# Performance work log

Measured on AMD Instinct MI355X. Metric: run time of the kernel, lower is better.

Reference implementation:

```python
import jax, jax.numpy as jnp
import numpy as np

OBS_SIZE = 128
ACTION_SIZE = 10
B = 64
T = 512
FEAT = 512          # HIDDEN_SIZE
H = 256             # HIDDEN_MEMORY_SIZE


def setup_inputs() -> dict:
    key = jax.random.key(0)
    ks = jax.random.split(key, 16)
    s = 0.05
    return {
        "obs": jax.random.normal(ks[0], (B, T, OBS_SIZE), jnp.float32),
        "action": jax.random.randint(ks[1], (B * T,), 0, ACTION_SIZE, jnp.int64 if jax.config.jax_enable_x64 else jnp.int32),
        "masks": jax.random.randint(ks[2], (B, T - 1), 0, 2, jnp.int32),
        "old_hidden_memory": jax.random.normal(ks[3], (B, 1, H), jnp.float32),
        # fnn: Linear(obs_size, 512) + ReLU
        "W1": jax.random.normal(ks[4], (FEAT, OBS_SIZE), jnp.float32) * s,
        "b1": jnp.zeros((FEAT,), jnp.float32),
        # GRU weights, PyTorch layout: gates ordered (r, z, n)
        "W_ih": jax.random.normal(ks[5], (3 * H, FEAT), jnp.float32) * s,
        "W_hh": jax.random.normal(ks[6], (3 * H, H), jnp.float32) * s,
        "b_ih": jnp.zeros((3 * H,), jnp.float32),
        "b_hh": jnp.zeros((3 * H,), jnp.float32),
        # actor / critic heads
        "Wa": jax.random.normal(ks[7], (ACTION_SIZE, H), jnp.float32) * s,
        "ba": jnp.zeros((ACTION_SIZE,), jnp.float32),
        "Wc": jax.random.normal(ks[8], (1, H), jnp.float32) * s,
        "bc": jnp.zeros((1,), jnp.float32),
    }


def _evaluate_action(obs, old_hidden_memory, W1, b1, W_ih, W_hh, b_ih, b_hh,
                     Wa, ba, Wc, bc, action, masks):
    # feature extractor: Linear + ReLU  [B,T,FEAT]
    feat = jax.nn.relu(jnp.einsum('bto,fo->btf', obs, W1) + b1)

    # Precompute input-side gate projections once: [T,B,3H]
    gx = jnp.einsum('btf,gf->tbg', feat, W_ih) + b_ih

    # mask sequence: prepend a column of ones, per the torch code -> [T,B]
    mask_seq = jnp.concatenate(
        [jnp.ones((1, B), jnp.float32), masks.astype(jnp.float32).T], axis=0)

    h0 = old_hidden_memory[:, 0]  # [B,H]

    def cell(h, inp):
        gx_t, m_t = inp
        h = h * m_t[:, None]                       # episode-reset masking
        gh = h @ W_hh.T + b_hh                     # [B,3H]
        r = jax.nn.sigmoid(gx_t[:, :H] + gh[:, :H])
        z = jax.nn.sigmoid(gx_t[:, H:2 * H] + gh[:, H:2 * H])
        n = jnp.tanh(gx_t[:, 2 * H:] + r * gh[:, 2 * H:])
        h_new = (1.0 - z) * n + z * h
        return h_new, h_new

    _, hs = jax.lax.scan(cell, h0, (gx, mask_seq))  # hs: [T,B,H]
    hs = hs.transpose(1, 0, 2).reshape(B * T, H)    # flatten(end_dim=1)

    logits = hs @ Wa.T + ba                         # [BT,A]
    logp = jax.nn.log_softmax(logits, axis=-1)
    log_prob = jnp.take_along_axis(logp, action[:, None].astype(jnp.int32), axis=1)[:, 0]
    entropy = -jnp.sum(jnp.exp(logp) * logp, axis=-1)
    value = hs @ Wc.T + bc                          # [BT,1]
    return value, log_prob, entropy


def reference(obs, action, masks, old_hidden_memory, W1, b1, W_ih, W_hh,
              b_ih, b_hh, Wa, ba, Wc, bc):
    return _evaluate_action(obs, old_hidden_memory, W1, b1, W_ih, W_hh,
                            b_ih, b_hh, Wa, ba, Wc, bc, action, masks)
```

## Files before the change

### kernel.cpp

```cpp
#include <hip/hip_runtime.h>
#include <hip/hip_fp16.h>
#include <stdint.h>

#define B_    64
#define T_    512
#define OBS_  128
#define FEAT_ 512
#define H_    256
#define G_    768
#define BT_   32768
#define NSLOT 16

typedef _Float16 f16x8 __attribute__((ext_vector_type(8)));
typedef float    f32x4 __attribute__((ext_vector_type(4)));

__device__ __forceinline__ uint32_t h2u(__half2 h){ union{ __half2 h; uint32_t u; } c; c.h = h; return c.u; }
__device__ __forceinline__ __half2 u2h(uint32_t u){ union{ uint32_t u; __half2 h; } c; c.u = u; return c.h; }

__device__ __forceinline__ int sw(int r, int c) { return r * 128 + ((c ^ (r & 7)) << 4); }

__device__ __forceinline__ uint4 cvt8(float4 a, float4 b) {
    uint4 u;
    u.x = h2u(__floats2half2_rn(a.x, a.y));
    u.y = h2u(__floats2half2_rn(a.z, a.w));
    u.z = h2u(__floats2half2_rn(b.x, b.y));
    u.w = h2u(__floats2half2_rn(b.z, b.w));
    return u;
}

__global__ __launch_bounds__(512, 4)
void fused_gemm(const float* __restrict__ obs, const uint4* __restrict__ W1f,
                const uint4* __restrict__ Wihf, const float* __restrict__ b1,
                const float* __restrict__ bih, uint32_t* __restrict__ gxC)
{
    __shared__ __align__(16) __half smem[16384];
    __half* obsA  = smem;
    __half* featL = smem + 8192;

    const int bid = blockIdx.x;
    const int m0 = (bid & 511) * 64;
    const int nt = bid >> 9;
    const int tid = threadIdx.x;
    const int lane = tid & 63, wn = tid >> 6;
    const int l15 = lane & 15, lq = lane >> 4;

    {
        const int r = tid >> 3, cpair = (tid & 7) * 2;
        #pragma unroll
        for (int c = 0; c < 2; ++c) {
            const int cc = cpair + c;
            const float* ap = obs + (size_t)(m0 + r) * OBS_ + cc * 8;
            const float4 f0 = ((const float4*)ap)[0];
            const float4 f1 = ((const float4*)ap)[1];
            *(uint4*)((char*)obsA + (cc >> 3) * 8192 + sw(r, cc & 7)) = cvt8(f0, f1);
        }
    }
    __syncthreads();

    f32x4 acc2[4][2];
    #pragma unroll
    for (int i = 0; i < 4; ++i)
        #pragma unroll
        for (int jj = 0; jj < 2; ++jj) { const f32x4 z = {0.f,0.f,0.f,0.f}; acc2[i][jj] = z; }

    for (int j = 0; j < 4; ++j) {
        uint4 w1f[4];
        {
            const uint4* base = W1f + ((size_t)(j * 8 + wn) * 4) * 64 + lane;
            #pragma unroll
            for (int q = 0; q < 4; ++q) w1f[q] = base[q * 64];
        }
        uint4 wif0[4];
        #pragma unroll
        for (int ni = 0; ni < 2; ++ni) {
            const uint4* base = Wihf + ((size_t)(nt * 16 + wn * 2 + ni) * 16 + j * 4) * 64 + lane;
            #pragma unroll
            for (int kc = 0; kc < 2; ++kc) wif0[ni * 2 + kc] = base[kc * 64];
        }
        f32x4 acc1[4];
        #pragma unroll
        for (int i = 0; i < 4; ++i) { const f32x4 z = {0.f,0.f,0.f,0.f}; acc1[i] = z; }
        #pragma unroll
        for (int kt = 0; kt < 2; ++kt)
            #pragma unroll
            for (int kc = 0; kc < 2; ++kc) {
                f16x8 af[4];
                #pragma unroll
                for (int mi = 0; mi < 4; ++mi)
                    af[mi] = *(const f16x8*)((const char*)obsA + kt * 8192 +
                                             sw(mi * 16 + l15, kc * 4 + lq));
                const f16x8 bf = *(const f16x8*)&w1f[kt * 2 + kc];
                #pragma unroll
                for (int mi = 0; mi < 4; ++mi)
                    acc1[mi] = __builtin_amdgcn_mfma_f32_16x16x32_f16(af[mi], bf, acc1[mi], 0, 0, 0);
            }
        {
            const int col = wn * 16 + l15;
            const float bv = b1[j * 128 + col];
            #pragma unroll
            for (int mi = 0; mi < 4; ++mi) {
                const f32x4 d = acc1[mi];
                #pragma unroll
                for (int rr = 0; rr < 4; ++rr) {
                    const float v = fmaxf(d[rr] + bv, 0.0f);
                    const uint32_t u = (uint32_t)__half_as_ushort(__float2half(v));
                    const uint32_t nb = (uint32_t)__shfl_xor((int)u, 1);
                    if (!(lane & 1)) {
                        const int row = mi * 16 + lq * 4 + rr;
                        *(uint32_t*)((char*)featL + (col >> 6) * 8192 + row * 128 +
                                     ((((col >> 3) & 7) ^ (row & 7)) << 4) + (col & 7) * 2) = u | (nb << 16);
                    }
                }
            }
        }
        __syncthreads();
        uint4 wif1[4];
        #pragma unroll
        for (int ni = 0; ni < 2; ++ni) {
            const uint4* base = Wihf + ((size_t)(nt * 16 + wn * 2 + ni) * 16 + j * 4 + 2) * 64 + lane;
            #pragma unroll
            for (int kc = 0; kc < 2; ++kc) wif1[ni * 2 + kc] = base[kc * 64];
        }
        #pragma unroll
        for (int kc = 0; kc < 2; ++kc) {
            f16x8 af[4];
            #pragma unroll
            for (int mi = 0; mi < 4; ++mi)
                af[mi] = *(const f16x8*)((const char*)featL +
                                         sw(mi * 16 + l15, kc * 4 + lq));
            #pragma unroll
            for (int ni = 0; ni < 2; ++ni) {
                const f16x8 bf = *(const f16x8*)&wif0[ni * 2 + kc];
                #pragma unroll
                for (int mi = 0; mi < 4; ++mi)
                    acc2[mi][ni] = __builtin_amdgcn_mfma_f32_16x16x32_f16(af[mi], bf, acc2[mi][ni], 0, 0, 0);
            }
        }
        #pragma unroll
        for (int kc = 0; kc < 2; ++kc) {
            f16x8 af[4];
            #pragma unroll
            for (int mi = 0; mi < 4; ++mi)
                af[mi] = *(const f16x8*)((const char*)featL + 8192 +
                                         sw(mi * 16 + l15, kc * 4 + lq));
            #pragma unroll
            for (int ni = 0; ni < 2; ++ni) {
                const f16x8 bf = *(const f16x8*)&wif1[ni * 2 + kc];
                #pragma unroll
                for (int mi = 0; mi < 4; ++mi)
                    acc2[mi][ni] = __builtin_amdgcn_mfma_f32_16x16x32_f16(af[mi], bf, acc2[mi][ni], 0, 0, 0);
            }
        }
        __syncthreads();
    }

    uint32_t* Cs = (uint32_t*)smem;
    #pragma unroll
    for (int ni = 0; ni < 2; ++ni) {
        const int col = wn * 32 + ni * 16 + l15;
        const float bv = bih[nt * 256 + col];
        #pragma unroll
        for (int mi = 0; mi < 4; ++mi) {
            const f32x4 d = acc2[mi][ni];
            #pragma unroll
            for (int rr = 0; rr < 4; ++rr) {
                const float v = d[rr] + bv;
                const uint32_t u = (uint32_t)__half_as_ushort(__float2half(v));
                const uint32_t nb = (uint32_t)__shfl_xor((int)u, 1);
                if (!(lane & 1))
                    Cs[(mi * 16 + lq * 4 + rr) * 128 + (col >> 1)] = u | (nb << 16);
            }
        }
    }
    __syncthreads();
    const int orow = tid >> 3, oseg = (tid & 7) * 16;
    #pragma unroll
    for (int c = 0; c < 4; ++c) {
        const uint4 val = *(const uint4*)&Cs[orow * 128 + oseg + c * 4];
        *(uint4*)(gxC + (size_t)(m0 + orow) * (G_ / 2) + (nt * 128) + oseg + c * 4) = val;
    }
}

template<int K>
__global__ void pack_bfrag(const float* __restrict__ W, uint32_t* __restrict__ out, int total)
{
    int p = blockIdx.x * 256 + threadIdx.x;
    if (p >= total) return;
    const int e2 = p & 3;
    const int l  = (p >> 2) & 63;
    const int f  = p >> 8;
    const int k32 = f & (K / 32 - 1);
    const int ct  = f / (K / 32);
    const int row = ct * 16 + (l & 15);
    const int k   = k32 * 32 + ((l >> 4) << 3) + e2 * 2;
    out[p] = h2u(__floats2half2_rn(W[(size_t)row * K + k], W[(size_t)row * K + k + 1]));
}

__global__ void pack_whh(const float* __restrict__ Whh, uint32_t* __restrict__ outR,
                         uint32_t* __restrict__ outL, int* __restrict__ qctl)
{
    if (blockIdx.x == 0 && threadIdx.x == 0) { qctl[0] = 0; qctl[1] = 0; }
    int p = blockIdx.x * 256 + threadIdx.x;
    if (p >= 512 * 192) return;
    const int v4 = p >> 2, sub = p & 3;
    const int t = v4 / 48, ic = v4 - t * 48;
    const int i = ic >> 3, c = ic & 7;
    const int w = t >> 6, lane = t & 63;
    const int row = w * 96 + i * 16 + (lane & 15);
    const int kb = c * 32 + ((lane >> 4) << 3) + sub * 2;
    const uint32_t val = h2u(__floats2half2_rn(Whh[row * 256 + kb], Whh[row * 256 + kb + 1]));
    if (c < 6) outR[(t * 36 + i * 6 + c) * 4 + sub] = val;
    else       outL[(((i << 1) + (c - 6)) * 512 + t) * 4 + sub] = val;
}

__global__ __launch_bounds__(512)
void seg_build(const int* __restrict__ masks, int* __restrict__ queue,
               int* __restrict__ qtail)
{
    __shared__ int sc[512];
    __shared__ int starts[512];
    __shared__ int cshr[2];
    const int b = blockIdx.x, s = threadIdx.x;
    const int is = (s == 0) || (masks[b * (T_ - 1) + s - 1] == 0);
    sc[s] = is;
    __syncthreads();
    #pragma unroll
    for (int off = 1; off < 512; off <<= 1) {
        int v = (s >= off) ? sc[s - off] : 0;
        __syncthreads();
        sc[s] += v;
        __syncthreads();
    }
    if (is) starts[sc[s] - 1] = s;
    if (s == 511) cshr[0] = sc[511];
    __syncthreads();
    const int cnt = cshr[0];
    int valid = 0, st = 0, ln = 0;
    if (s < cnt) {
        st = starts[s];
        const int nxt = (s + 1 < cnt) ? starts[s + 1] : T_;
        ln = nxt - st;
        valid = (st == 0 || ln >= 2) ? 1 : 0;
    }
    sc[s] = valid;
    __syncthreads();
    #pragma unroll
    for (int off = 1; off < 512; off <<= 1) {
        int v = (s >= off) ? sc[s - off] : 0;
        __syncthreads();
        sc[s] += v;
        __syncthreads();
    }
    if (s == 511) cshr[1] = atomicAdd(qtail, sc[511]);
    __syncthreads();
    if (valid) queue[cshr[1] + sc[s] - 1] = (b << 19) | (st << 10) | ln;
}

__global__ __launch_bounds__(256)
void h0pre(const __half* __restrict__ gx, const float* __restrict__ bhh,
           const int* __restrict__ masks, uint32_t* __restrict__ hs2)
{
    for (int row = blockIdx.x; row < B_ * (T_ - 1); row += gridDim.x) {
        if (masks[row] != 0) continue;
        const int b = row / (T_ - 1), t = 1 + row - b * (T_ - 1);
        const int e = threadIdx.x;
        const __half* grow = gx + (size_t)(b * T_ + t) * 768;
        const float gxr = __half2float(grow[e]);
        const float gxz = __half2float(grow[e + 256]);
        const float gxn = __half2float(grow[e + 512]);
        const float rg = 1.f / (1.f + exp2f(-(gxr + bhh[e]) * 1.44269504f));
        const float zg = 1.f / (1.f + exp2f(-(gxz + bhh[e + 256]) * 1.44269504f));
        const float nin = gxn + rg * bhh[e + 512];
        const float e2x = exp2f(nin * 2.885390082f);
        const float ng = 1.f - 2.f / (e2x + 1.f);
        const float hnew = (1.f - zg) * ng;
        const float other = __shfl_xor(hnew, 1);
        if (!(e & 1)) hs2[(size_t)(b * T_ + t) * 128 + (e >> 1)] = h2u(__floats2half2_rn(hnew, other));
    }
}

__global__ __launch_bounds__(512, 2)
void gru_mfma(const __half* __restrict__ gx, const uint4* __restrict__ WhhR,
              const uint4* __restrict__ WhhL, const float* __restrict__ bhh,
              const float* __restrict__ h0, const int* __restrict__ queue,
              const int* __restrict__ qctl, uint32_t* __restrict__ hs2)
{
    __shared__ __align__(16) __half Hl[NSLOT * 256];
    __shared__ __align__(16) __half Plh[NSLOT * 784];
    __shared__ __align__(16) uint4  Wl[12 * 512];
    __shared__ float Bl[G_];
    __shared__ int s_end[NSLOT], s_row[NSLOT], s_act[NSLOT], s_nxt[NSLOT];
    __shared__ int cur;

    const int tid = threadIdx.x;
    const int lane = tid & 63, w = tid >> 6;
    const int s = tid >> 5, g32 = tid & 31, e0 = g32 * 8;
    const int col = lane & 15, lq = lane >> 4;

    f16x8 wr[36];
    {
        const f16x8* wp = (const f16x8*)(WhhR + (size_t)tid * 36);
        #pragma unroll
        for (int i = 0; i < 36; ++i) wr[i] = wp[i];
    }
    #pragma unroll
    for (int i = 0; i < 12; ++i) Wl[i * 512 + tid] = WhhL[i * 512 + tid];
    if (tid < 384) { Bl[tid] = bhh[tid]; Bl[tid + 384] = bhh[tid + 384]; }
    { const uint4 z4 = {0u, 0u, 0u, 0u}; *(uint4*)((char*)Hl + tid * 16) = z4; }

    const int NQ = qctl[0];
    const int gb = blockIdx.x;
    const int lo = (int)(((long long)NQ * gb) >> 8);
    const int hi = (int)(((long long)NQ * (gb + 1)) >> 8);
    if (tid == 0) cur = lo + NSLOT;
    __syncthreads();

    {
        int e = -1;
        if (lo + s < hi) e = queue[lo + s];
        if (e >= 0) {
            const int ln = e & 1023, st = (e >> 10) & 511, nb = e >> 19;
            uint4 hseed;
            if (st == 0) {
                const float4 a = *(const float4*)(h0 + nb * 256 + e0);
                const float4 b = *(const float4*)(h0 + nb * 256 + e0 + 4);
                hseed = cvt8(a, b);
                if (g32 == 0) { s_row[s] = nb * T_; s_end[s] = nb * T_ + ln; }
            } else {
                hseed = *(const uint4*)(hs2 + (size_t)(nb * T_ + st) * 128 + g32 * 4);
                if (g32 == 0) { s_row[s] = nb * T_ + st + 1; s_end[s] = nb * T_ + st + ln; }
            }
            *(uint4*)((char*)Hl + s * 512 + ((g32 ^ (s & 7)) << 4)) = hseed;
            if (g32 == 0) {
                s_act[s] = 1;
                const int p = atomicAdd(&cur, 1);
                s_nxt[s] = (p < hi) ? queue[p] : -1;
            }
        } else if (g32 == 0) {
            s_act[s] = 0; s_nxt[s] = -1; s_row[s] = 0; s_end[s] = 0;
        }
    }
    __syncthreads();

    for (;;) {
        bool alive = false;
        #pragma unroll
        for (int i = 0; i < NSLOT; ++i) alive |= (s_act[i] != 0);
        if (!alive) break;

        const int myrow = s_row[s];
        const int nxte = s_nxt[s];
        const __half* grow = gx + (size_t)myrow * G_;
        const f16x8 gr = *(const f16x8*)(grow + e0);
        const f16x8 gz = *(const f16x8*)(grow + 256 + e0);
        const f16x8 gn = *(const f16x8*)(grow + 512 + e0);
        uint4 su = {0u, 0u, 0u, 0u};
        if (nxte >= 0) {
            const int st = (nxte >> 10) & 511, nb = nxte >> 19;
            if (st == 0) {
                const float4 a = *(const float4*)(h0 + nb * 256 + e0);
                const float4 b = *(const float4*)(h0 + nb * 256 + e0 + 4);
                su = cvt8(a, b);
            } else {
                su = *(const uint4*)(hs2 + (size_t)(nb * T_ + st) * 128 + g32 * 4);
            }
        }
        f16x8 bfv[8];
        #pragma unroll
        for (int c = 0; c < 8; ++c)
            bfv[c] = *(const f16x8*)((const char*)Hl + col * 512 +
                                     ((((c << 2) + lq) ^ (col & 7)) << 4));
        f32x4 acc[6];
        #pragma unroll
        for (int i = 0; i < 6; ++i) { const f32x4 z = {0.f, 0.f, 0.f, 0.f}; acc[i] = z; }
        #pragma unroll
        for (int c = 0; c < 6; ++c)
            #pragma unroll
            for (int i = 0; i < 6; ++i)
                acc[i] = __builtin_amdgcn_mfma_f32_16x16x32_f16(wr[i * 6 + c], bfv[c], acc[i], 0, 0, 0);
        #pragma unroll
        for (int c2 = 0; c2 < 2; ++c2)
            #pragma unroll
            for (int i = 0; i < 6; ++i) {
                const f16x8 wlt = *(const f16x8*)&Wl[(i * 2 + c2) * 512 + tid];
                acc[i] = __builtin_amdgcn_mfma_f32_16x16x32_f16(wlt, bfv[6 + c2], acc[i], 0, 0, 0);
            }
        #pragma unroll
        for (int i = 0; i < 6; ++i) {
            uint2 ph;
            ph.x = h2u(__floats2half2_rn(acc[i][0], acc[i][1]));
            ph.y = h2u(__floats2half2_rn(acc[i][2], acc[i][3]));
            *(uint2*)(Plh + col * 784 + (w * 96 + i * 16 + lq * 4)) = ph;
        }
        asm volatile("s_waitcnt lgkmcnt(0)" ::: "memory");
        __builtin_amdgcn_s_barrier();

        if (s_act[s]) {
            const __half* Pr = Plh + s * 784;
            const f16x8 R  = *(const f16x8*)(Pr + e0);
            const f16x8 Z  = *(const f16x8*)(Pr + 256 + e0);
            const f16x8 Nn = *(const f16x8*)(Pr + 512 + e0);
            const f32x4 br0 = *(const f32x4*)(Bl + e0),       br1 = *(const f32x4*)(Bl + e0 + 4);
            const f32x4 bz0 = *(const f32x4*)(Bl + 256 + e0), bz1 = *(const f32x4*)(Bl + 256 + e0 + 4);
            const f32x4 bn0 = *(const f32x4*)(Bl + 512 + e0), bn1 = *(const f32x4*)(Bl + 512 + e0 + 4);
            const uint4 hp4 = *(const uint4*)((const char*)Hl + s * 512 + ((g32 ^ (s & 7)) << 4));
            const __half2 q0 = u2h(hp4.x), q1 = u2h(hp4.y), q2 = u2h(hp4.z), q3 = u2h(hp4.w);
            const float hpv[8] = { __low2float(q0), __high2float(q0), __low2float(q1), __high2float(q1),
                                   __low2float(q2), __high2float(q2), __low2float(q3), __high2float(q3) };
            float hn[8];
            #pragma unroll
            for (int j = 0; j < 8; ++j) {
                const float ghr = (float)R[j]  + (j < 4 ? br0[j] : br1[j - 4]);
                const float ghz = (float)Z[j]  + (j < 4 ? bz0[j] : bz1[j - 4]);
                const float ghn = (float)Nn[j] + (j < 4 ? bn0[j] : bn1[j - 4]);
                const float rg = 1.f / (1.f + exp2f(-((float)gr[j] + ghr) * 1.44269504f));
                const float zg = 1.f / (1.f + exp2f(-((float)gz[j] + ghz) * 1.44269504f));
                const float nin = (float)gn[j] + rg * ghn;
                const float ex = exp2f(nin * 2.885390082f);
                const float ng = 1.f - 2.f / (ex + 1.f);
                hn[j] = (1.f - zg) * ng + zg * hpv[j];
            }
            uint4 hp;
            hp.x = h2u(__floats2half2_rn(hn[0], hn[1]));
            hp.y = h2u(__floats2half2_rn(hn[2], hn[3]));
            hp.z = h2u(__floats2half2_rn(hn[4], hn[5]));
            hp.w = h2u(__floats2half2_rn(hn[6], hn[7]));
            *(uint4*)(hs2 + (size_t)myrow * 128 + g32 * 4) = hp;
            if (myrow + 1 < s_end[s]) {
                *(uint4*)((char*)Hl + s * 512 + ((g32 ^ (s & 7)) << 4)) = hp;
                if (g32 == 0) s_row[s] = myrow + 1;
            } else if (nxte >= 0) {
                const int ln = nxte & 1023, st = (nxte >> 10) & 511, nb = nxte >> 19;
                *(uint4*)((char*)Hl + s * 512 + ((g32 ^ (s & 7)) << 4)) = su;
                if (g32 == 0) {
                    if (st == 0) { s_row[s] = nb * T_;          s_end[s] = nb * T_ + ln; }
                    else         { s_row[s] = nb * T_ + st + 1; s_end[s] = nb * T_ + st + ln; }
                    const int p = atomicAdd(&cur, 1);
                    s_nxt[s] = (p < hi) ? queue[p] : -1;
                }
            } else if (g32 == 0) {
                s_act[s] = 0;
            }
        }
        asm volatile("s_waitcnt lgkmcnt(0)" ::: "memory");
        __builtin_amdgcn_s_barrier();
    }
}

__global__ __launch_bounds__(256)
void heads_kernel(const uint32_t* __restrict__ hs2, const float* __restrict__ Wa,
                  const float* __restrict__ ba, const float* __restrict__ Wc,
                  const float* __restrict__ bc, const int* __restrict__ action,
                  float* __restrict__ out)
{
    const int wid = threadIdx.x >> 6, lane = threadIdx.x & 63;
    const int row = blockIdx.x * 4 + wid;
    const uint2 hv2 = ((const uint2*)(hs2 + (size_t)row * 128))[lane];
    const __half2 ha = u2h(hv2.x), hb = u2h(hv2.y);
    const float h0f = __low2float(ha), h1f = __high2float(ha);
    const float h2f = __low2float(hb), h3f = __high2float(hb);
    float sums[11];
    #pragma unroll
    for (int n = 0; n < 11; ++n) {
        const float* wrow = (n < 10) ? (Wa + n * 256) : Wc;
        const float4 wv = ((const float4*)wrow)[lane];
        sums[n] = h0f * wv.x + h1f * wv.y + h2f * wv.z + h3f * wv.w;
    }
    #pragma unroll
    for (int n = 0; n < 11; ++n) {
        float v = sums[n];
        #pragma unroll
        for (int off = 32; off; off >>= 1) v += __shfl_xor(v, off);
        sums[n] = v;
    }
    float logits[10];
    #pragma unroll
    for (int n = 0; n < 10; ++n) logits[n] = sums[n] + ba[n];
    const float value = sums[10] + bc[0];
    float mx = logits[0];
    #pragma unroll
    for (int n = 1; n < 10; ++n) mx = fmaxf(mx, logits[n]);
    float ssum = 0.f, sdot = 0.f;
    #pragma unroll
    for (int n = 0; n < 10; ++n) {
        float d = logits[n] - mx;
        float e = exp2f(d * 1.44269504f);
        ssum += e; sdot += e * d;
    }
    const float lns = logf(ssum);
    const float lse = mx + lns;
    const float entropy = lns - sdot / ssum;
    const int a = action[row];
    float la = 0.f;
    #pragma unroll
    for (int n = 0; n < 10; ++n) la = (n == a) ? logits[n] : la;
    if (lane == 0) {
        out[row] = value;
        out[BT_ + row] = la - lse;
        out[2 * BT_ + row] = entropy;
    }
}

extern "C" void kernel_launch(void* const* d_in, const int* in_sizes, int n_in,
                              void* d_out, int out_size, void* d_ws, size_t ws_size,
                              hipStream_t stream)
{
    const float* obs    = (const float*)d_in[0];
    const int*   action = (const int*)d_in[1];
    const int*   masks  = (const int*)d_in[2];
    const float* h0     = (const float*)d_in[3];
    const float* W1     = (const float*)d_in[4];
    const float* b1     = (const float*)d_in[5];
    const float* Wih    = (const float*)d_in[6];
    const float* Whh    = (const float*)d_in[7];
    const float* bih    = (const float*)d_in[8];
    const float* bhh    = (const float*)d_in[9];
    const float* Wa     = (const float*)d_in[10];
    const float* ba     = (const float*)d_in[11];
    const float* Wc     = (const float*)d_in[12];
    const float* bc     = (const float*)d_in[13];
    float* out = (float*)d_out;

    char* p = (char*)d_ws;
    __half*   gx   = (__half*)p;    p += (size_t)BT_ * G_ * 2;
    uint32_t* hs2  = (uint32_t*)p;  p += (size_t)BT_ * H_ * 2;
    uint32_t* W1f  = (uint32_t*)p;  p += FEAT_ * OBS_ * 2;
    uint32_t* Wihf = (uint32_t*)p;  p += G_ * FEAT_ * 2;
    uint4*    WhhR = (uint4*)p;     p += 512 * 36 * 16;
    uint4*    WhhL = (uint4*)p;     p += 12 * 512 * 16;
    int*      queue= (int*)p;       p += B_ * 512 * 4;
    int*      qctl = (int*)p;       p += 256;

    pack_bfrag<OBS_><<<128, 256, 0, stream>>>(W1, W1f, FEAT_ * OBS_ / 2);
    pack_bfrag<FEAT_><<<768, 256, 0, stream>>>(Wih, Wihf, G_ * FEAT_ / 2);
    pack_whh<<<384, 256, 0, stream>>>(Whh, (uint32_t*)WhhR, (uint32_t*)WhhL, qctl);
    seg_build<<<B_, 512, 0, stream>>>(masks, queue, &qctl[0]);
    fused_gemm<<<1536, 512, 0, stream>>>(obs, (const uint4*)W1f, (const uint4*)Wihf, b1, bih, (uint32_t*)gx);
    h0pre<<<2048, 256, 0, stream>>>(gx, bhh, masks, hs2);
    gru_mfma<<<256, 512, 0, stream>>>(gx, WhhR, WhhL, bhh, h0, queue, qctl, hs2);
    heads_kernel<<<8192, 256, 0, stream>>>(hs2, Wa, ba, Wc, bc, action, out);
}
```

Measured before the change: 177.5 us.

## Double-buffer feature tile, prefetch weights, and merge weight-packing kernels

The fused GEMM now alternates between two shared-memory feature buffers, which removes the trailing barrier in each chunk loop. It also issues the next chunk's W1 and W_ih fragment loads early so they overlap with the current MFMA work. The three weight-packing kernels are merged into one launch to cut launch overhead. Shared memory per block grows from 32 KB to 48 KB, which may lower occupancy at 4 blocks per CU, and the prefetched fragments raise register pressure.

New measurement: 187.9 us. 1.06x slower.

```diff
diff --git a/kernel.cpp b/kernel.cpp
--- a/kernel.cpp
+++ b/kernel.cpp
@@ -33,7 +33,7 @@
                 const uint4* __restrict__ Wihf, const float* __restrict__ b1,
                 const float* __restrict__ bih, uint32_t* __restrict__ gxC)
 {
-    __shared__ __align__(16) __half smem[16384];
+    __shared__ __align__(16) __half smem[24576];
     __half* obsA  = smem;
     __half* featL = smem + 8192;
 
@@ -63,20 +63,22 @@
         #pragma unroll
         for (int jj = 0; jj < 2; ++jj) { const f32x4 z = {0.f,0.f,0.f,0.f}; acc2[i][jj] = z; }
 
+    uint4 w1f[4], wif0[4], wif1[4];
+    {
+        const uint4* base1 = W1f + ((size_t)(0 * 8 + wn) * 4) * 64 + lane;
+        #pragma unroll
+        for (int q = 0; q < 4; ++q) w1f[q] = base1[q * 64];
+        #pragma unroll
+        for (int ni = 0; ni < 2; ++ni) {
+            const uint4* base = Wihf + ((size_t)(nt * 16 + wn * 2 + ni) * 16 + 0) * 64 + lane;
+            #pragma unroll
+            for (int kc = 0; kc < 2; ++kc) wif0[ni * 2 + kc] = base[kc * 64];
+        }
+    }
+
+    #pragma unroll
     for (int j = 0; j < 4; ++j) {
-        uint4 w1f[4];
-        {
-            const uint4* base = W1f + ((size_t)(j * 8 + wn) * 4) * 64 + lane;
-            #pragma unroll
-            for (int q = 0; q < 4; ++q) w1f[q] = base[q * 64];
-        }
-        uint4 wif0[4];
-        #pragma unroll
-        for (int ni = 0; ni < 2; ++ni) {
-            const uint4* base = Wihf + ((size_t)(nt * 16 + wn * 2 + ni) * 16 + j * 4) * 64 + lane;
-            #pragma unroll
-            for (int kc = 0; kc < 2; ++kc) wif0[ni * 2 + kc] = base[kc * 64];
-        }
+        char* fbuf = (char*)featL + (j & 1) * 16384;
         f32x4 acc1[4];
         #pragma unroll
         for (int i = 0; i < 4; ++i) { const f32x4 z = {0.f,0.f,0.f,0.f}; acc1[i] = z; }
@@ -107,14 +109,18 @@
                     const uint32_t nb = (uint32_t)__shfl_xor((int)u, 1);
                     if (!(lane & 1)) {
                         const int row = mi * 16 + lq * 4 + rr;
-                        *(uint32_t*)((char*)featL + (col >> 6) * 8192 + row * 128 +
+                        *(uint32_t*)(fbuf + (col >> 6) * 8192 + row * 128 +
                                      ((((col >> 3) & 7) ^ (row & 7)) << 4) + (col & 7) * 2) = u | (nb << 16);
                     }
                 }
             }
         }
         __syncthreads();
-        uint4 wif1[4];
+        if (j < 3) {
+            const uint4* base1 = W1f + ((size_t)((j + 1) * 8 + wn) * 4) * 64 + lane;
+            #pragma unroll
+            for (int q = 0; q < 4; ++q) w1f[q] = base1[q * 64];
+        }
         #pragma unroll
         for (int ni = 0; ni < 2; ++ni) {
             const uint4* base = Wihf + ((size_t)(nt * 16 + wn * 2 + ni) * 16 + j * 4 + 2) * 64 + lane;
@@ -126,8 +132,7 @@
             f16x8 af[4];
             #pragma unroll
             for (int mi = 0; mi < 4; ++mi)
-                af[mi] = *(const f16x8*)((const char*)featL +
-                                         sw(mi * 16 + l15, kc * 4 + lq));
+                af[mi] = *(const f16x8*)(fbuf + sw(mi * 16 + l15, kc * 4 + lq));
             #pragma unroll
             for (int ni = 0; ni < 2; ++ni) {
                 const f16x8 bf = *(const f16x8*)&wif0[ni * 2 + kc];
@@ -136,13 +141,20 @@
                     acc2[mi][ni] = __builtin_amdgcn_mfma_f32_16x16x32_f16(af[mi], bf, acc2[mi][ni], 0, 0, 0);
             }
         }
+        if (j < 3) {
+            #pragma unroll
+            for (int ni = 0; ni < 2; ++ni) {
+                const uint4* base = Wihf + ((size_t)(nt * 16 + wn * 2 + ni) * 16 + (j + 1) * 4) * 64 + lane;
+                #pragma unroll
+                for (int kc = 0; kc < 2; ++kc) wif0[ni * 2 + kc] = base[kc * 64];
+            }
+        }
         #pragma unroll
         for (int kc = 0; kc < 2; ++kc) {
             f16x8 af[4];
             #pragma unroll
             for (int mi = 0; mi < 4; ++mi)
-                af[mi] = *(const f16x8*)((const char*)featL + 8192 +
-                                         sw(mi * 16 + l15, kc * 4 + lq));
+                af[mi] = *(const f16x8*)(fbuf + 8192 + sw(mi * 16 + l15, kc * 4 + lq));
             #pragma unroll
             for (int ni = 0; ni < 2; ++ni) {
                 const f16x8 bf = *(const f16x8*)&wif1[ni * 2 + kc];
@@ -151,9 +163,9 @@
                     acc2[mi][ni] = __builtin_amdgcn_mfma_f32_16x16x32_f16(af[mi], bf, acc2[mi][ni], 0, 0, 0);
             }
         }
-        __syncthreads();
-    }
-
+    }
+
+    __syncthreads();
     uint32_t* Cs = (uint32_t*)smem;
     #pragma unroll
     for (int ni = 0; ni < 2; ++ni) {
@@ -181,36 +193,40 @@
     }
 }
 
-template<int K>
-__global__ void pack_bfrag(const float* __restrict__ W, uint32_t* __restrict__ out, int total)
-{
-    int p = blockIdx.x * 256 + threadIdx.x;
-    if (p >= total) return;
-    const int e2 = p & 3;
-    const int l  = (p >> 2) & 63;
-    const int f  = p >> 8;
-    const int k32 = f & (K / 32 - 1);
-    const int ct  = f / (K / 32);
-    const int row = ct * 16 + (l & 15);
-    const int k   = k32 * 32 + ((l >> 4) << 3) + e2 * 2;
-    out[p] = h2u(__floats2half2_rn(W[(size_t)row * K + k], W[(size_t)row * K + k + 1]));
-}
-
-__global__ void pack_whh(const float* __restrict__ Whh, uint32_t* __restrict__ outR,
-                         uint32_t* __restrict__ outL, int* __restrict__ qctl)
-{
-    if (blockIdx.x == 0 && threadIdx.x == 0) { qctl[0] = 0; qctl[1] = 0; }
-    int p = blockIdx.x * 256 + threadIdx.x;
-    if (p >= 512 * 192) return;
-    const int v4 = p >> 2, sub = p & 3;
-    const int t = v4 / 48, ic = v4 - t * 48;
-    const int i = ic >> 3, c = ic & 7;
-    const int w = t >> 6, lane = t & 63;
-    const int row = w * 96 + i * 16 + (lane & 15);
-    const int kb = c * 32 + ((lane >> 4) << 3) + sub * 2;
-    const uint32_t val = h2u(__floats2half2_rn(Whh[row * 256 + kb], Whh[row * 256 + kb + 1]));
-    if (c < 6) outR[(t * 36 + i * 6 + c) * 4 + sub] = val;
-    else       outL[(((i << 1) + (c - 6)) * 512 + t) * 4 + sub] = val;
+__global__ __launch_bounds__(256)
+void prep_all(const float* __restrict__ W1, const float* __restrict__ Wih,
+              const float* __restrict__ Whh, uint32_t* __restrict__ W1f,
+              uint32_t* __restrict__ Wihf, uint32_t* __restrict__ WhhR,
+              uint32_t* __restrict__ WhhL, int* __restrict__ qctl)
+{
+    const int bx = blockIdx.x;
+    if (bx == 0 && threadIdx.x == 0) { qctl[0] = 0; qctl[1] = 0; }
+    if (bx < 128) {
+        const int p = bx * 256 + threadIdx.x;
+        const int e2 = p & 3, l = (p >> 2) & 63, f = p >> 8;
+        const int k32 = f & 3, ct = f >> 2;
+        const int row = ct * 16 + (l & 15);
+        const int k = k32 * 32 + ((l >> 4) << 3) + e2 * 2;
+        W1f[p] = h2u(__floats2half2_rn(W1[(size_t)row * OBS_ + k], W1[(size_t)row * OBS_ + k + 1]));
+    } else if (bx < 896) {
+        const int p = (bx - 128) * 256 + threadIdx.x;
+        const int e2 = p & 3, l = (p >> 2) & 63, f = p >> 8;
+        const int k32 = f & 15, ct = f >> 4;
+        const int row = ct * 16 + (l & 15);
+        const int k = k32 * 32 + ((l >> 4) << 3) + e2 * 2;
+        Wihf[p] = h2u(__floats2half2_rn(Wih[(size_t)row * FEAT_ + k], Wih[(size_t)row * FEAT_ + k + 1]));
+    } else {
+        const int p = (bx - 896) * 256 + threadIdx.x;
+        const int v4 = p >> 2, sub = p & 3;
+        const int t = v4 / 48, ic = v4 - t * 48;
+        const int i = ic >> 3, c = ic & 7;
+        const int w = t >> 6, lane = t & 63;
+        const int row = w * 96 + i * 16 + (lane & 15);
+        const int kb = c * 32 + ((lane >> 4) << 3) + sub * 2;
+        const uint32_t val = h2u(__floats2half2_rn(Whh[row * 256 + kb], Whh[row * 256 + kb + 1]));
+        if (c < 6) WhhR[(t * 36 + i * 6 + c) * 4 + sub] = val;
+        else       WhhL[(((i << 1) + (c - 6)) * 512 + t) * 4 + sub] = val;
+    }
 }
 
 __global__ __launch_bounds__(512)
@@ -531,9 +547,8 @@
     int*      queue= (int*)p;       p += B_ * 512 * 4;
     int*      qctl = (int*)p;       p += 256;
 
-    pack_bfrag<OBS_><<<128, 256, 0, stream>>>(W1, W1f, FEAT_ * OBS_ / 2);
-    pack_bfrag<FEAT_><<<768, 256, 0, stream>>>(Wih, Wihf, G_ * FEAT_ / 2);
-    pack_whh<<<384, 256, 0, stream>>>(Whh, (uint32_t*)WhhR, (uint32_t*)WhhL, qctl);
+    prep_all<<<1280, 256, 0, stream>>>(W1, Wih, Whh, W1f, Wihf,
+                                       (uint32_t*)WhhR, (uint32_t*)WhhL, qctl);
     seg_build<<<B_, 512, 0, stream>>>(masks, queue, &qctl[0]);
     fused_gemm<<<1536, 512, 0, stream>>>(obs, (const uint4*)W1f, (const uint4*)Wihf, b1, bih, (uint32_t*)gx);
     h0pre<<<2048, 256, 0, stream>>>(gx, bhh, masks, hs2);
```
